# Kernel tuning notes

Hardware: AMD Instinct MI355X
Metric: run time of the kernel (lower is better)

## Reference

```python
import jax, jax.numpy as jnp
from jax import lax
import numpy as np

B, S, D_IN, D_OUT, LAT, N_STATE = 8, 2048, 1024, 1024, 256, 32
D_INNER, D_CONV, DT_RANK, N_BLK = 2 * D_OUT, 4, D_OUT // 16, 2


def setup_inputs() -> dict:
    key = jax.random.key(0)
    ks = iter(jax.random.split(key, 24))
    r = lambda shp, s=0.02: jax.random.normal(next(ks), shp, dtype=jnp.float32) * s
    inp = {
        "x": jax.random.normal(next(ks), (B, S, D_IN), dtype=jnp.float32),
        "W_in": r((D_IN, D_OUT)), "b_in": jnp.zeros((D_OUT,), jnp.float32),
        "Wa1": r((D_OUT, LAT)), "ba1": jnp.zeros((LAT,), jnp.float32),
        "Wa2": r((LAT, LAT)), "ba2": jnp.zeros((LAT,), jnp.float32),
        # per-block params, leading axis = N_BLK
        "gamma": jnp.ones((N_BLK, D_OUT), jnp.float32),
        "in_proj_w": r((N_BLK, D_OUT, 2 * D_INNER)),
        "conv_w": r((N_BLK, D_INNER, D_CONV), 0.1),
        "conv_b": jnp.zeros((N_BLK, D_INNER), jnp.float32),
        "x_proj_w": r((N_BLK, D_INNER, DT_RANK + 2 * N_STATE)),
        "dt_proj_w": r((N_BLK, DT_RANK, D_INNER), 0.1),
        "dt_proj_b": jnp.full((N_BLK, D_INNER), -4.6, jnp.float32),  # softplus(-4.6)~0.01
        "A_log": jnp.log(jnp.broadcast_to(jnp.arange(1, N_STATE + 1, dtype=jnp.float32), (N_BLK, D_INNER, N_STATE))),
        "D": jnp.ones((N_BLK, D_INNER), jnp.float32),
        "out_proj_w": r((N_BLK, D_INNER, D_OUT)),
    }
    return inp


def rms_norm(x, gamma):
    # F.normalize(x, dim=-1) * sqrt(d) * gamma
    norm = jnp.sqrt(jnp.sum(x * x, axis=-1, keepdims=True))
    return x / jnp.maximum(norm, 1e-12) * (x.shape[-1] ** 0.5) * gamma


def causal_conv1d(x, w, b):
    # x: [b, d, L], w: [d, d_conv] depthwise, causal (left) padding
    y = lax.conv_general_dilated(
        x, w[:, None, :], window_strides=(1,), padding=[(D_CONV - 1, 0)],
        feature_group_count=x.shape[1], dimension_numbers=("NCH", "OIH", "NCH"))
    return y + b[None, :, None]


def selective_scan(dA, dBu, C):
    # dA, dBu: [b, L, d_inner, n], C: [b, L, n] -> y: [b, L, d_inner]
    def step(h, inp):
        dA_t, dBu_t, C_t = inp
        h = dA_t * h + dBu_t
        return h, jnp.einsum("bdn,bn->bd", h, C_t)
    h0 = jnp.zeros(dA.shape[:1] + dA.shape[2:], dA.dtype)
    _, ys = lax.scan(step, h0, (dA.swapaxes(0, 1), dBu.swapaxes(0, 1), C.swapaxes(0, 1)))
    return ys.swapaxes(0, 1)


def mamba(u, in_w, cw, cb, xw, dtw, dtb, A_log, Dp, ow):
    # u: [b, L, d_model]
    xz = u @ in_w                              # [b, L, 2*d_inner]
    xh, z = jnp.split(xz, 2, axis=-1)
    xh = causal_conv1d(xh.swapaxes(1, 2), cw, cb).swapaxes(1, 2)
    xh = jax.nn.silu(xh)                       # [b, L, d_inner]
    xdbc = xh @ xw                             # [b, L, dt_rank + 2n]
    dt, Bm, Cm = jnp.split(xdbc, [DT_RANK, DT_RANK + N_STATE], axis=-1)
    dt = jax.nn.softplus(dt @ dtw + dtb)       # [b, L, d_inner]
    A = -jnp.exp(A_log)                        # [d_inner, n]
    dA = jnp.exp(dt[..., None] * A)            # [b, L, d_inner, n]
    dBu = dt[..., None] * Bm[:, :, None, :] * xh[..., None]
    y = selective_scan(dA, dBu, Cm) + Dp * xh
    y = y * jax.nn.silu(z)
    return y @ ow


def reference(x, W_in, b_in, Wa1, ba1, Wa2, ba2, gamma, in_proj_w, conv_w,
              conv_b, x_proj_w, dt_proj_w, dt_proj_b, A_log, D, out_proj_w):
    out = x @ W_in + b_in                      # [b, s, d]
    length = out.shape[1]
    w = jax.nn.silu(out @ Wa1 + ba1) @ Wa2 + ba2   # [b, s, LAT]
    w1 = jax.nn.softmax(w, axis=-1) * (LAT / length)
    w2 = jax.nn.softmax(w, axis=-2)
    weights = (w1 + w2) * 0.5
    out = jnp.einsum("bsd,bsS->bSd", out, weights)  # [b, LAT, d]
    for i in range(N_BLK):  # residual RMSNorm + Mamba (dropout = identity in eval)
        out = out + mamba(rms_norm(out, gamma[i]), in_proj_w[i], conv_w[i],
                          conv_b[i], x_proj_w[i], dt_proj_w[i], dt_proj_b[i],
                          A_log[i], D[i], out_proj_w[i])
    return out
```

## Files before the change

kernel.cpp:

```cpp
#include <hip/hip_runtime.h>
#include <math.h>
#include <stdint.h>

#define BB 8
#define SS 2048
#define D_IN 1024
#define D_OUTC 1024
#define LATC 256
#define NSTATE 32
#define DINNER 2048
#define DCONV 4
#define DTRANK 64
#define NCH 32

__device__ __forceinline__ float silu_f(float v) { return v * (1.f / (1.f + __expf(-v))); }
__device__ __forceinline__ float softplus_f(float v) {
    return fmaxf(v, 0.f) + log1pf(__expf(-fabsf(v)));
}

typedef short short8 __attribute__((ext_vector_type(8)));
typedef float f32x4 __attribute__((ext_vector_type(4)));

__device__ __forceinline__ unsigned short f2bf(float f) {
    unsigned u = __builtin_bit_cast(unsigned, f);
    u += 0x7FFFu + ((u >> 16) & 1u);
    return (unsigned short)(u >> 16);
}
__device__ __forceinline__ int pack2(float a, float b) {
    return (int)((unsigned)f2bf(a) | ((unsigned)f2bf(b) << 16));
}

typedef const __attribute__((address_space(1))) unsigned int* gas_ptr;
typedef __attribute__((address_space(3))) unsigned int* las_ptr;
__device__ __forceinline__ void gload16(const void* g, void* l) {
    __builtin_amdgcn_global_load_lds(
        reinterpret_cast<gas_ptr>(reinterpret_cast<uintptr_t>(g)),
        reinterpret_cast<las_ptr>(reinterpret_cast<uintptr_t>(l)),
        16, 0, 0);
}

__global__ __launch_bounds__(256) void transp_bf(const float* __restrict__ src,
                                                 unsigned short* __restrict__ dst,
                                                 int K, int N, long zsrc, long zdst)
{
    __shared__ float tile[32][33];
    src += (size_t)blockIdx.z * zsrc;
    dst += (size_t)blockIdx.z * zdst;
    const int n0 = blockIdx.x * 32;
    const int k0 = blockIdx.y * 32;
    const int x = threadIdx.x & 31;
    const int y = threadIdx.x >> 5;
#pragma unroll
    for (int j = 0; j < 4; j++)
        tile[y + 8 * j][x] = src[(size_t)(k0 + y + 8 * j) * N + n0 + x];
    __syncthreads();
#pragma unroll
    for (int j = 0; j < 4; j++)
        dst[(size_t)(n0 + y + 8 * j) * K + k0 + x] = f2bf(tile[x][y + 8 * j]);
}

__global__ __launch_bounds__(256) void transp16(const unsigned short* __restrict__ src,
                                                unsigned short* __restrict__ dst,
                                                int K, int N, long zsrc, long zdst)
{
    __shared__ unsigned short tile[32][33];
    src += (size_t)blockIdx.z * zsrc;
    dst += (size_t)blockIdx.z * zdst;
    const int n0 = blockIdx.x * 32;
    const int k0 = blockIdx.y * 32;
    const int x = threadIdx.x & 31;
    const int y = threadIdx.x >> 5;
#pragma unroll
    for (int j = 0; j < 4; j++)
        tile[y + 8 * j][x] = src[(size_t)(k0 + y + 8 * j) * N + n0 + x];
    __syncthreads();
#pragma unroll
    for (int j = 0; j < 4; j++)
        dst[(size_t)(n0 + y + 8 * j) * K + k0 + x] = tile[x][y + 8 * j];
}

__global__ __launch_bounds__(256) void cvt_bf16(const float* __restrict__ in,
                                                unsigned short* __restrict__ out)
{
    size_t i = ((size_t)blockIdx.x * 256 + threadIdx.x) * 8;
    float4 a = *(const float4*)(in + i);
    float4 b = *(const float4*)(in + i + 4);
    int4 w;
    w.x = pack2(a.x, a.y); w.y = pack2(a.z, a.w);
    w.z = pack2(b.x, b.y); w.w = pack2(b.z, b.w);
    *(int4*)(out + i) = w;
}

__global__ __launch_bounds__(256) void gemm16(
    const unsigned short* __restrict__ A, int lda,
    const unsigned short* __restrict__ BT, int ldb,
    const float* __restrict__ bias,
    float* __restrict__ C, int ldc,
    unsigned short* __restrict__ C16, int ldc16,
    int M, int N, int K, int act, int accum,
    int kspl, long zA, long zB, long zC, long zK)
{
    __shared__ __align__(16) unsigned short As[2][128 * 32];
    __shared__ __align__(16) unsigned short Bs[2][128 * 32];

    const int bz = blockIdx.z / kspl;
    const int ks = blockIdx.z % kspl;
    A += (size_t)bz * zA + (size_t)ks * (size_t)K;
    BT += (size_t)bz * zB + (size_t)ks * (size_t)K;
    if (C) C += (size_t)bz * zC + (size_t)ks * zK;

    const int tid = threadIdx.x;
    const int lane = tid & 63;
    const int wave = tid >> 6;
    const int wr = wave >> 1;
    const int wc = wave & 1;
    const int quad = lane >> 4;
    const int l16 = lane & 15;

    const int nbx = gridDim.x;
    const int nwg = nbx * gridDim.y;
    const int orig = blockIdx.y * nbx + blockIdx.x;
    const int q = nwg >> 3, r = nwg & 7;
    const int xcd = orig & 7, lid = orig >> 3;
    const int swz = (xcd < r) ? (xcd * (q + 1) + lid)
                              : (r * (q + 1) + (xcd - r) * q + lid);
    const int m0 = (swz / nbx) * 128;
    const int n0 = (swz % nbx) * 128;

    const int srow4 = lane >> 2;
    const int sphys = lane & 3;

    f32x4 acc[4][4];
#pragma unroll
    for (int i = 0; i < 4; i++)
#pragma unroll
        for (int j = 0; j < 4; j++) acc[i][j] = (f32x4){0.f, 0.f, 0.f, 0.f};

    const int nt = K >> 5;

    auto STAGE = [&](int buf, int t) {
        const int k0 = t << 5;
#pragma unroll
        for (int i = 0; i < 2; i++) {
            const int rbase = (wave << 5) + (i << 4);
            const int rr = rbase + srow4;
            const int ls = sphys ^ ((rr >> 1) & 3);
            gload16(A + (size_t)(m0 + rr) * lda + (k0 + (ls << 3)), &As[buf][rbase << 5]);
            gload16(BT + (size_t)(n0 + rr) * ldb + (k0 + (ls << 3)), &Bs[buf][rbase << 5]);
        }
    };

    STAGE(0, 0);
    asm volatile("s_waitcnt vmcnt(0)" ::: "memory");
    __syncthreads();

    int cur = 0;
    for (int t = 0; t < nt; ++t) {
        if (t + 1 < nt) STAGE(cur ^ 1, t + 1);

        short8 af[4], bfr[4];
#pragma unroll
        for (int i = 0; i < 4; i++) {
            const int ar = (wr << 6) + (i << 4) + l16;
            af[i] = *(const short8*)&As[cur][(ar << 5) + ((quad ^ ((ar >> 1) & 3)) << 3)];
            const int br = (wc << 6) + (i << 4) + l16;
            bfr[i] = *(const short8*)&Bs[cur][(br << 5) + ((quad ^ ((br >> 1) & 3)) << 3)];
        }
#pragma unroll
        for (int i = 0; i < 4; i++)
#pragma unroll
            for (int j = 0; j < 4; j++)
                acc[i][j] = __builtin_amdgcn_mfma_f32_16x16x32_bf16(af[i], bfr[j], acc[i][j], 0, 0, 0);

        asm volatile("s_waitcnt vmcnt(0)" ::: "memory");
        __syncthreads();
        cur ^= 1;
    }

#pragma unroll
    for (int j = 0; j < 4; j++) {
        int gn = n0 + wc * 64 + j * 16 + l16;
        float bv = bias ? bias[gn] : 0.f;
#pragma unroll
        for (int i = 0; i < 4; i++) {
#pragma unroll
            for (int r2 = 0; r2 < 4; r2++) {
                int gm = m0 + wr * 64 + i * 16 + quad * 4 + r2;
                float v = acc[i][j][r2] + bv;
                if (act == 1) v = silu_f(v);
                else if (act == 2) v = softplus_f(v);
                if (C) {
                    size_t ci = (size_t)gm * ldc + gn;
                    if (accum) C[ci] += v;
                    else C[ci] = v;
                }
                if (C16) C16[(size_t)gm * ldc16 + gn] = f2bf(v);
            }
        }
    }
}

__global__ __launch_bounds__(256) void gemm_kernel(
    const float* __restrict__ A, int lda, long strideA,
    const float* __restrict__ B, int ldb, long strideB,
    const float* __restrict__ bias,
    float* __restrict__ C, int ldc, long strideC,
    int M, int N, int K, int transA, int act, int accum)
{
    __shared__ float As[16][65];
    __shared__ float Bsh[16][64];

    const int bz = blockIdx.z;
    const float* Ab = A + (size_t)bz * strideA;
    const float* Bb = B + (size_t)bz * strideB;
    float* Cb = C + (size_t)bz * strideC;

    const int tx = threadIdx.x;
    const int ty = threadIdx.y;
    const int tid = ty * 16 + tx;
    const int m0 = blockIdx.y * 64;
    const int n0 = blockIdx.x * 64;

    float acc[4][4];
#pragma unroll
    for (int i = 0; i < 4; i++)
#pragma unroll
        for (int j = 0; j < 4; j++) acc[i][j] = 0.f;

    for (int k0 = 0; k0 < K; k0 += 16) {
        if (!transA) {
            int row = tid >> 2;
            int kc = (tid & 3) * 4;
            int gm = m0 + row;
#pragma unroll
            for (int j = 0; j < 4; j++) {
                int gk = k0 + kc + j;
                As[kc + j][row] = (gm < M && gk < K) ? Ab[(size_t)gm * lda + gk] : 0.f;
            }
        } else {
            int krow = tid >> 4;
            int mc = (tid & 15) * 4;
            int gk = k0 + krow;
#pragma unroll
            for (int j = 0; j < 4; j++) {
                int gm = m0 + mc + j;
                As[krow][mc + j] = (gm < M && gk < K) ? Ab[(size_t)gk * lda + gm] : 0.f;
            }
        }
        {
            int krow = tid >> 4;
            int nc = (tid & 15) * 4;
            int gk = k0 + krow;
#pragma unroll
            for (int j = 0; j < 4; j++) {
                int gn = n0 + nc + j;
                Bsh[krow][nc + j] = (gk < K && gn < N) ? Bb[(size_t)gk * ldb + gn] : 0.f;
            }
        }
        __syncthreads();
#pragma unroll
        for (int k = 0; k < 16; k++) {
            float a[4], bv[4];
#pragma unroll
            for (int i = 0; i < 4; i++) a[i] = As[k][ty * 4 + i];
#pragma unroll
            for (int j = 0; j < 4; j++) bv[j] = Bsh[k][tx * 4 + j];
#pragma unroll
            for (int i = 0; i < 4; i++)
#pragma unroll
                for (int j = 0; j < 4; j++) acc[i][j] += a[i] * bv[j];
        }
        __syncthreads();
    }

#pragma unroll
    for (int i = 0; i < 4; i++) {
        int gm = m0 + ty * 4 + i;
        if (gm >= M) continue;
#pragma unroll
        for (int j = 0; j < 4; j++) {
            int gn = n0 + tx * 4 + j;
            if (gn >= N) continue;
            float v = acc[i][j];
            if (bias) v += bias[gn];
            if (act == 1) v = silu_f(v);
            else if (act == 2) v = softplus_f(v);
            size_t ci = (size_t)gm * ldc + gn;
            if (accum) Cb[ci] += v;
            else Cb[ci] = v;
        }
    }
}

__global__ __launch_bounds__(256) void merge4_kernel(const float* __restrict__ part,
                                                     float* __restrict__ out, int n)
{
    int i = blockIdx.x * 256 + threadIdx.x;
    out[i] = part[i] + part[i + n] + part[i + 2 * n] + part[i + 3 * n];
}

__global__ __launch_bounds__(256) void merge2_kernel(const float* __restrict__ part,
                                                     float* __restrict__ out, int n)
{
    int i = blockIdx.x * 256 + threadIdx.x;
    out[i] = part[i] + part[i + n];
}

__global__ __launch_bounds__(256) void colstats_part_kernel(const float* __restrict__ w,
                                                            float* __restrict__ part)
{
    int b = blockIdx.x / NCH;
    int ch = blockIdx.x % NCH;
    int l = threadIdx.x;
    const float* base = w + ((size_t)b * SS + (size_t)ch * (SS / NCH)) * LATC + l;
    float m = -1e30f, s = 0.f;
    for (int t = 0; t < SS / NCH; t++) {
        float v = base[(size_t)t * LATC];
        float nm = fmaxf(m, v);
        s = s * __expf(m - nm) + __expf(v - nm);
        m = nm;
    }
    float2* p = (float2*)part;
    p[(size_t)(b * LATC + l) * NCH + ch] = make_float2(m, s);
}

__global__ __launch_bounds__(256) void colstats_merge_kernel(const float* __restrict__ part,
                                                             float* __restrict__ colst)
{
    int idx = blockIdx.x * 256 + threadIdx.x;
    const float2* p = (const float2*)part + (size_t)idx * NCH;
    float m = -1e30f, s = 0.f;
#pragma unroll 4
    for (int c = 0; c < NCH; c++) {
        float2 v = p[c];
        float nm = fmaxf(m, v.x);
        s = s * __expf(m - nm) + v.y * __expf(v.x - nm);
        m = nm;
    }
    colst[idx * 2] = m;
    colst[idx * 2 + 1] = s;
}

__global__ __launch_bounds__(256) void softmix_kernel(float* __restrict__ w,
                                                      const float* __restrict__ colst)
{
    int bs = blockIdx.x;
    int b = bs / SS;
    int l = threadIdx.x;
    float* row = w + (size_t)bs * LATC;
    float v = row[l];

    __shared__ float sm[256];
    sm[l] = v;
    __syncthreads();
    for (int st = 128; st > 0; st >>= 1) {
        if (l < st) sm[l] = fmaxf(sm[l], sm[l + st]);
        __syncthreads();
    }
    float rmax = sm[0];
    __syncthreads();
    float e = __expf(v - rmax);
    sm[l] = e;
    __syncthreads();
    for (int st = 128; st > 0; st >>= 1) {
        if (l < st) sm[l] += sm[l + st];
        __syncthreads();
    }
    float rsum = sm[0];

    float w1 = e / rsum * ((float)LATC / (float)SS);
    float cm = colst[(b * LATC + l) * 2];
    float cs = colst[(b * LATC + l) * 2 + 1];
    float w2 = __expf(v - cm) / cs;
    row[l] = 0.5f * (w1 + w2);
}

__global__ __launch_bounds__(256) void rmsnorm_kernel(const float* __restrict__ x,
                                                      const float* __restrict__ gamma,
                                                      unsigned short* __restrict__ out)
{
    int row = blockIdx.x;
    const float* xr = x + (size_t)row * D_OUTC;
    float v[4];
    float ss = 0.f;
#pragma unroll
    for (int i = 0; i < 4; i++) {
        v[i] = xr[threadIdx.x + i * 256];
        ss += v[i] * v[i];
    }
#pragma unroll
    for (int off = 32; off >= 1; off >>= 1) ss += __shfl_xor(ss, off, 64);
    __shared__ float sred[4];
    int wave = threadIdx.x >> 6;
    if ((threadIdx.x & 63) == 0) sred[wave] = ss;
    __syncthreads();
    float tot = sred[0] + sred[1] + sred[2] + sred[3];
    float inv = 32.0f / fmaxf(sqrtf(tot), 1e-12f);
    unsigned short* outr = out + (size_t)row * D_OUTC;
#pragma unroll
    for (int i = 0; i < 4; i++) {
        int d = threadIdx.x + i * 256;
        outr[d] = f2bf(v[i] * inv * gamma[d]);
    }
}

__global__ __launch_bounds__(256) void conv_silu_kernel(const float* __restrict__ xz,
                                                        const float* __restrict__ cw,
                                                        const float* __restrict__ cb,
                                                        float* __restrict__ xh, int L)
{
    int idx = blockIdx.x * 256 + threadIdx.x;
    int c = idx % DINNER;
    int bl = idx / DINNER;
    int l = bl % L;
    int b = bl / L;
    float acc = cb[c];
#pragma unroll
    for (int j = 0; j < DCONV; j++) {
        int ls = l - (DCONV - 1) + j;
        if (ls >= 0)
            acc += xz[((size_t)(b * L + ls)) * (2 * DINNER) + c] * cw[c * DCONV + j];
    }
    xh[idx] = silu_f(acc);
}

#define SCH 4
__global__ __launch_bounds__(256) void scan_kernel(const float* __restrict__ dty,
                                                   const float* __restrict__ xh,
                                                   const float* __restrict__ xz,
                                                   const float* __restrict__ xdbc,
                                                   const float* __restrict__ A_log,
                                                   const float* __restrict__ Dp,
                                                   unsigned short* __restrict__ ybf,
                                                   int L)
{
    const int t = threadIdx.x;
    const int g = t & 7;
    const int dloc = t >> 3;
    const int b = blockIdx.x >> 6;
    const int d = ((blockIdx.x & 63) << 5) + dloc;

    float4 Av = *(const float4*)(A_log + (size_t)d * NSTATE + g * 4);
    const float A0 = -__expf(Av.x), A1 = -__expf(Av.y), A2 = -__expf(Av.z), A3 = -__expf(Av.w);
    float h0 = 0.f, h1 = 0.f, h2 = 0.f, h3 = 0.f;
    const float Dd = Dp[d];

    const float* pdt = dty + (size_t)b * L * DINNER + d;
    const float* pxh = xh + (size_t)b * L * DINNER + d;
    const float* pz  = xz + (size_t)b * L * 2 * DINNER + DINNER + d;
    const float* pbc = xdbc + (size_t)b * L * 128 + DTRANK + g * 4;
    unsigned short* pout = ybf + (size_t)b * L * DINNER + d;

    float a_dt[SCH], a_x[SCH], a_z[SCH];
    float4 a_B[SCH], a_C[SCH];
    float n_dt[SCH], n_x[SCH], n_z[SCH];
    float4 n_B[SCH], n_C[SCH];

#pragma unroll
    for (int j = 0; j < SCH; j++) {
        a_dt[j] = pdt[(size_t)j * DINNER];
        a_x[j]  = pxh[(size_t)j * DINNER];
        a_z[j]  = pz[(size_t)j * 2 * DINNER];
        a_B[j]  = *(const float4*)(pbc + (size_t)j * 128);
        a_C[j]  = *(const float4*)(pbc + (size_t)j * 128 + NSTATE);
    }

    for (int l0 = 0; l0 < L; l0 += SCH) {
        const int lb = (l0 + SCH < L) ? (l0 + SCH) : l0;
#pragma unroll
        for (int j = 0; j < SCH; j++) {
            n_dt[j] = pdt[(size_t)(lb + j) * DINNER];
            n_x[j]  = pxh[(size_t)(lb + j) * DINNER];
            n_z[j]  = pz[(size_t)(lb + j) * 2 * DINNER];
            n_B[j]  = *(const float4*)(pbc + (size_t)(lb + j) * 128);
            n_C[j]  = *(const float4*)(pbc + (size_t)(lb + j) * 128 + NSTATE);
        }
#pragma unroll
        for (int j = 0; j < SCH; j++) {
            float dtv = a_dt[j], xv = a_x[j], zv = a_z[j];
            float dtx = dtv * xv;
            float e0 = __expf(dtv * A0);
            float e1 = __expf(dtv * A1);
            float e2 = __expf(dtv * A2);
            float e3 = __expf(dtv * A3);
            h0 = e0 * h0 + dtx * a_B[j].x;
            h1 = e1 * h1 + dtx * a_B[j].y;
            h2 = e2 * h2 + dtx * a_B[j].z;
            h3 = e3 * h3 + dtx * a_B[j].w;
            float accv = h0 * a_C[j].x + h1 * a_C[j].y + h2 * a_C[j].z + h3 * a_C[j].w;
            accv += __shfl_xor(accv, 1, 64);
            accv += __shfl_xor(accv, 2, 64);
            accv += __shfl_xor(accv, 4, 64);
            if (g == 0) {
                float yv = (accv + Dd * xv) * silu_f(zv);
                pout[(size_t)(l0 + j) * DINNER] = f2bf(yv);
            }
        }
#pragma unroll
        for (int j = 0; j < SCH; j++) {
            a_dt[j] = n_dt[j]; a_x[j] = n_x[j]; a_z[j] = n_z[j];
            a_B[j] = n_B[j];   a_C[j] = n_C[j];
        }
    }
}


extern "C" void kernel_launch(void* const* d_in, const int* in_sizes, int n_in,
                              void* d_out, int out_size, void* d_ws, size_t ws_size,
                              hipStream_t stream)
{
    const float* x      = (const float*)d_in[0];
    const float* W_in   = (const float*)d_in[1];
    const float* b_in   = (const float*)d_in[2];
    const float* Wa1    = (const float*)d_in[3];
    const float* ba1    = (const float*)d_in[4];
    const float* Wa2    = (const float*)d_in[5];
    const float* ba2    = (const float*)d_in[6];
    const float* gamma  = (const float*)d_in[7];
    const float* in_w   = (const float*)d_in[8];
    const float* conv_w = (const float*)d_in[9];
    const float* conv_b = (const float*)d_in[10];
    const float* x_w    = (const float*)d_in[11];
    const float* dt_w   = (const float*)d_in[12];
    const float* dt_b   = (const float*)d_in[13];
    const float* A_log  = (const float*)d_in[14];
    const float* Dp     = (const float*)d_in[15];
    const float* out_w  = (const float*)d_in[16];
    float* latout = (float*)d_out;

    char* wsb = (char*)d_ws;
    const size_t MB = 1 << 20;

    unsigned short* out0_bf = (unsigned short*)(wsb);
    unsigned short* xbf     = (unsigned short*)(wsb + 32 * MB);
    float*          wbuf    = (float*)(wsb + 64 * MB);
    unsigned short* t1_bf   = (unsigned short*)(wsb + 80 * MB);
    unsigned short* WinT    = (unsigned short*)(wsb + 88 * MB);
    unsigned short* Wa1T    = (unsigned short*)(wsb + 90 * MB);
    unsigned short* Wa2T    = (unsigned short*)(wsb + 90 * MB + 512 * 1024);
    float*          cs_part = (float*)(wsb + 91 * MB);
    float*          colst   = (float*)(wsb + 95 * MB);

    unsigned short* out0T   = (unsigned short*)(wsb + 32 * MB);
    unsigned short* wT      = (unsigned short*)(wsb + 80 * MB);
    float*          part6   = (float*)(wsb + 64 * MB);

    unsigned short* unorm_bf  = (unsigned short*)(wsb);
    float*          xdbc_part = (float*)(wsb + 4 * MB);
    float*          dtbuf     = (float*)(wsb + 8 * MB);
    unsigned short* ybf       = (unsigned short*)(wsb + 24 * MB);
    float*          xz        = (float*)(wsb + 32 * MB);
    float*          xh        = (float*)(wsb + 64 * MB);
    unsigned short* wprojT    = (unsigned short*)(wsb + 80 * MB);
    unsigned short* oprojT    = (unsigned short*)(wsb + 88 * MB);
    float*          xdbc      = (float*)(wsb + 92 * MB);

    dim3 blk(16, 16);
    const int L = LATC;
    const int M1 = BB * SS;
    const int ML = BB * L;

    cvt_bf16<<<dim3((size_t)M1 * D_IN / 2048), dim3(256), 0, stream>>>(x, xbf);
    transp_bf<<<dim3(D_OUTC / 32, D_IN / 32), dim3(256), 0, stream>>>(W_in, WinT, D_IN, D_OUTC, 0, 0);
    transp_bf<<<dim3(LATC / 32, D_OUTC / 32), dim3(256), 0, stream>>>(Wa1, Wa1T, D_OUTC, LATC, 0, 0);
    transp_bf<<<dim3(LATC / 32, LATC / 32), dim3(256), 0, stream>>>(Wa2, Wa2T, LATC, LATC, 0, 0);

    gemm16<<<dim3(D_OUTC / 128, M1 / 128), dim3(256), 0, stream>>>(
        xbf, D_IN, WinT, D_IN, b_in, (float*)nullptr, 0, out0_bf, D_OUTC,
        M1, D_OUTC, D_IN, 0, 0, 1, 0, 0, 0, 0);

    gemm16<<<dim3(LATC / 128, M1 / 128), dim3(256), 0, stream>>>(
        out0_bf, D_OUTC, Wa1T, D_OUTC, ba1, (float*)nullptr, 0, t1_bf, LATC,
        M1, LATC, D_OUTC, 1, 0, 1, 0, 0, 0, 0);

    gemm16<<<dim3(LATC / 128, M1 / 128), dim3(256), 0, stream>>>(
        t1_bf, LATC, Wa2T, LATC, ba2, wbuf, LATC, (unsigned short*)nullptr, 0,
        M1, LATC, LATC, 0, 0, 1, 0, 0, 0, 0);

    colstats_part_kernel<<<dim3(BB * NCH), dim3(256), 0, stream>>>(wbuf, cs_part);
    colstats_merge_kernel<<<dim3(BB * LATC / 256), dim3(256), 0, stream>>>(cs_part, colst);
    softmix_kernel<<<dim3(BB * SS), dim3(256), 0, stream>>>(wbuf, colst);

    transp16<<<dim3(D_OUTC / 32, SS / 32, BB), dim3(256), 0, stream>>>(
        out0_bf, out0T, SS, D_OUTC, (long)SS * D_OUTC, (long)D_OUTC * SS);
    transp_bf<<<dim3(LATC / 32, SS / 32, BB), dim3(256), 0, stream>>>(
        wbuf, wT, SS, LATC, (long)SS * LATC, (long)LATC * SS);
    gemm16<<<dim3(D_OUTC / 128, LATC / 128, BB * 2), dim3(256), 0, stream>>>(
        wT, SS, out0T, SS, (const float*)nullptr,
        part6, D_OUTC, (unsigned short*)nullptr, 0,
        LATC, D_OUTC, SS / 2, 0, 0,
        2, (long)LATC * SS, (long)D_OUTC * SS, (long)LATC * D_OUTC,
        (long)BB * LATC * D_OUTC);
    merge2_kernel<<<dim3(BB * LATC * D_OUTC / 256), dim3(256), 0, stream>>>(
        part6, latout, BB * LATC * D_OUTC);

    for (int i = 0; i < 2; i++) {
        const float* in_wi = in_w + (size_t)i * D_OUTC * 2 * DINNER;
        const float* cwi = conv_w + (size_t)i * DINNER * DCONV;
        const float* cbi = conv_b + (size_t)i * DINNER;
        const float* xwi = x_w + (size_t)i * DINNER * (DTRANK + 2 * NSTATE);
        const float* dtwi = dt_w + (size_t)i * DTRANK * DINNER;
        const float* dtbi = dt_b + (size_t)i * DINNER;
        const float* Ali = A_log + (size_t)i * DINNER * NSTATE;
        const float* Dpi = Dp + (size_t)i * DINNER;
        const float* owi = out_w + (size_t)i * DINNER * D_OUTC;
        const float* gi = gamma + (size_t)i * D_OUTC;

        transp_bf<<<dim3(2 * DINNER / 32, D_OUTC / 32), dim3(256), 0, stream>>>(
            in_wi, wprojT, D_OUTC, 2 * DINNER, 0, 0);
        transp_bf<<<dim3(D_OUTC / 32, DINNER / 32), dim3(256), 0, stream>>>(
            owi, oprojT, DINNER, D_OUTC, 0, 0);

        rmsnorm_kernel<<<dim3(ML), dim3(256), 0, stream>>>(latout, gi, unorm_bf);

        gemm16<<<dim3(2 * DINNER / 128, ML / 128), dim3(256), 0, stream>>>(
            unorm_bf, D_OUTC, wprojT, D_OUTC, (const float*)nullptr,
            xz, 2 * DINNER, (unsigned short*)nullptr, 0,
            ML, 2 * DINNER, D_OUTC, 0, 0, 1, 0, 0, 0, 0);

        conv_silu_kernel<<<dim3(BB * L * DINNER / 256), dim3(256), 0, stream>>>(xz, cwi, cbi, xh, L);

        gemm_kernel<<<dim3(128 / 64, ML / 64, 4), blk, 0, stream>>>(
            xh, DINNER, 512, xwi, 128, (long)512 * 128, (const float*)nullptr,
            xdbc_part, 128, (long)ML * 128, ML, 128, 512, 0, 0, 0);
        merge4_kernel<<<dim3(ML * 128 / 256), dim3(256), 0, stream>>>(
            xdbc_part, xdbc, ML * 128);

        gemm_kernel<<<dim3(DINNER / 64, ML / 64, 1), blk, 0, stream>>>(
            xdbc, 128, 0, dtwi, DINNER, 0, dtbi, dtbuf, DINNER, 0, ML, DINNER, DTRANK, 0, 2, 0);

        scan_kernel<<<dim3(BB * DINNER * 8 / 256), dim3(256), 0, stream>>>(
            dtbuf, xh, xz, xdbc, Ali, Dpi, ybf, L);

        gemm16<<<dim3(D_OUTC / 128, ML / 128), dim3(256), 0, stream>>>(
            ybf, DINNER, oprojT, DINNER, (const float*)nullptr,
            latout, D_OUTC, (unsigned short*)nullptr, 0,
            ML, D_OUTC, DINNER, 0, 1, 1, 0, 0, 0, 0);
    }
}
```

Measured before the change: 995.7 us.

## Split selective scan into chunked three-pass parallel scan over sequence

The sequential scan over the 256-step latent sequence is replaced by three passes. The first computes per-chunk final states and summed dt for 4 chunks in parallel. A small kernel then propagates the carried states across chunks. The scan is re-run per chunk starting from the propagated state. This gives 4x more blocks and a 4x shorter serial dependency chain, at the cost of reading dt/x/B twice and extra launches. Scratch buffers reuse workspace regions that held the in-proj weights and the normalized input.

```diff
diff --git a/kernel.cpp b/kernel.cpp
--- a/kernel.cpp
+++ b/kernel.cpp
@@ -425,12 +425,104 @@
 }
 
 #define SCH 4
+#define NCHS 4
+#define CHL (LATC / NCHS)
+
+__global__ __launch_bounds__(256) void scan_prop(const float* __restrict__ dty,
+                                                 const float* __restrict__ xh,
+                                                 const float* __restrict__ xdbc,
+                                                 const float* __restrict__ A_log,
+                                                 float* __restrict__ hfin,
+                                                 float* __restrict__ sdtb,
+                                                 int L)
+{
+    const int t = threadIdx.x;
+    const int g = t & 7;
+    const int dloc = t >> 3;
+    const int b = blockIdx.x >> 6;
+    const int d = ((blockIdx.x & 63) << 5) + dloc;
+    const int c = blockIdx.y;
+
+    float4 Av = *(const float4*)(A_log + (size_t)d * NSTATE + g * 4);
+    const float A0 = -__expf(Av.x), A1 = -__expf(Av.y), A2 = -__expf(Av.z), A3 = -__expf(Av.w);
+    float h0 = 0.f, h1 = 0.f, h2 = 0.f, h3 = 0.f, sdt = 0.f;
+
+    const float* pdt = dty + ((size_t)b * L + (size_t)c * CHL) * DINNER + d;
+    const float* pxh = xh + ((size_t)b * L + (size_t)c * CHL) * DINNER + d;
+    const float* pbc = xdbc + ((size_t)b * L + (size_t)c * CHL) * 128 + DTRANK + g * 4;
+
+    float a_dt[SCH], a_x[SCH];
+    float4 a_B[SCH];
+    float n_dt[SCH], n_x[SCH];
+    float4 n_B[SCH];
+
+#pragma unroll
+    for (int j = 0; j < SCH; j++) {
+        a_dt[j] = pdt[(size_t)j * DINNER];
+        a_x[j]  = pxh[(size_t)j * DINNER];
+        a_B[j]  = *(const float4*)(pbc + (size_t)j * 128);
+    }
+
+    for (int l0 = 0; l0 < CHL; l0 += SCH) {
+        const int lb = (l0 + SCH < CHL) ? (l0 + SCH) : l0;
+#pragma unroll
+        for (int j = 0; j < SCH; j++) {
+            n_dt[j] = pdt[(size_t)(lb + j) * DINNER];
+            n_x[j]  = pxh[(size_t)(lb + j) * DINNER];
+            n_B[j]  = *(const float4*)(pbc + (size_t)(lb + j) * 128);
+        }
+#pragma unroll
+        for (int j = 0; j < SCH; j++) {
+            float dtv = a_dt[j];
+            float dtx = dtv * a_x[j];
+            sdt += dtv;
+            float e0 = __expf(dtv * A0);
+            float e1 = __expf(dtv * A1);
+            float e2 = __expf(dtv * A2);
+            float e3 = __expf(dtv * A3);
+            h0 = e0 * h0 + dtx * a_B[j].x;
+            h1 = e1 * h1 + dtx * a_B[j].y;
+            h2 = e2 * h2 + dtx * a_B[j].z;
+            h3 = e3 * h3 + dtx * a_B[j].w;
+        }
+#pragma unroll
+        for (int j = 0; j < SCH; j++) {
+            a_dt[j] = n_dt[j]; a_x[j] = n_x[j]; a_B[j] = n_B[j];
+        }
+    }
+
+    float4 hv; hv.x = h0; hv.y = h1; hv.z = h2; hv.w = h3;
+    *(float4*)(hfin + ((((size_t)b * NCHS + c) * DINNER + d) << 5) + g * 4) = hv;
+    if (g == 0) sdtb[((size_t)b * NCHS + c) * DINNER + d] = sdt;
+}
+
+__global__ __launch_bounds__(256) void scan_mid(float* __restrict__ hfin,
+                                                const float* __restrict__ sdtb,
+                                                const float* __restrict__ A_log)
+{
+    int idx = blockIdx.x * 256 + threadIdx.x;
+    int n = idx & 31;
+    int d = (idx >> 5) & (DINNER - 1);
+    int b = idx >> 16;
+    float An = -__expf(A_log[(size_t)d * NSTATE + n]);
+    float h = 0.f;
+#pragma unroll
+    for (int c = 0; c < NCHS; c++) {
+        size_t slot = ((((size_t)b * NCHS + c) * DINNER + d) << 5) + n;
+        float hf = hfin[slot];
+        hfin[slot] = h;
+        float S = sdtb[((size_t)b * NCHS + c) * DINNER + d];
+        h = __expf(An * S) * h + hf;
+    }
+}
+
 __global__ __launch_bounds__(256) void scan_kernel(const float* __restrict__ dty,
                                                    const float* __restrict__ xh,
                                                    const float* __restrict__ xz,
                                                    const float* __restrict__ xdbc,
                                                    const float* __restrict__ A_log,
                                                    const float* __restrict__ Dp,
+                                                   const float* __restrict__ hin,
                                                    unsigned short* __restrict__ ybf,
                                                    int L)
 {
@@ -439,17 +531,19 @@
     const int dloc = t >> 3;
     const int b = blockIdx.x >> 6;
     const int d = ((blockIdx.x & 63) << 5) + dloc;
+    const int c = blockIdx.y;
 
     float4 Av = *(const float4*)(A_log + (size_t)d * NSTATE + g * 4);
     const float A0 = -__expf(Av.x), A1 = -__expf(Av.y), A2 = -__expf(Av.z), A3 = -__expf(Av.w);
-    float h0 = 0.f, h1 = 0.f, h2 = 0.f, h3 = 0.f;
+    float4 hv = *(const float4*)(hin + ((((size_t)b * NCHS + c) * DINNER + d) << 5) + g * 4);
+    float h0 = hv.x, h1 = hv.y, h2 = hv.z, h3 = hv.w;
     const float Dd = Dp[d];
 
-    const float* pdt = dty + (size_t)b * L * DINNER + d;
-    const float* pxh = xh + (size_t)b * L * DINNER + d;
-    const float* pz  = xz + (size_t)b * L * 2 * DINNER + DINNER + d;
-    const float* pbc = xdbc + (size_t)b * L * 128 + DTRANK + g * 4;
-    unsigned short* pout = ybf + (size_t)b * L * DINNER + d;
+    const float* pdt = dty + ((size_t)b * L + (size_t)c * CHL) * DINNER + d;
+    const float* pxh = xh + ((size_t)b * L + (size_t)c * CHL) * DINNER + d;
+    const float* pz  = xz + ((size_t)b * L + (size_t)c * CHL) * 2 * DINNER + DINNER + d;
+    const float* pbc = xdbc + ((size_t)b * L + (size_t)c * CHL) * 128 + DTRANK + g * 4;
+    unsigned short* pout = ybf + ((size_t)b * L + (size_t)c * CHL) * DINNER + d;
 
     float a_dt[SCH], a_x[SCH], a_z[SCH];
     float4 a_B[SCH], a_C[SCH];
@@ -465,8 +559,8 @@
         a_C[j]  = *(const float4*)(pbc + (size_t)j * 128 + NSTATE);
     }
 
-    for (int l0 = 0; l0 < L; l0 += SCH) {
-        const int lb = (l0 + SCH < L) ? (l0 + SCH) : l0;
+    for (int l0 = 0; l0 < CHL; l0 += SCH) {
+        const int lb = (l0 + SCH < CHL) ? (l0 + SCH) : l0;
 #pragma unroll
         for (int j = 0; j < SCH; j++) {
             n_dt[j] = pdt[(size_t)(lb + j) * DINNER];
@@ -554,6 +648,8 @@
     unsigned short* wprojT    = (unsigned short*)(wsb + 80 * MB);
     unsigned short* oprojT    = (unsigned short*)(wsb + 88 * MB);
     float*          xdbc      = (float*)(wsb + 92 * MB);
+    float*          hfin      = (float*)(wsb + 80 * MB);
+    float*          sdtb      = (float*)(wsb);
 
     dim3 blk(16, 16);
     const int L = LATC;
@@ -629,8 +725,12 @@
         gemm_kernel<<<dim3(DINNER / 64, ML / 64, 1), blk, 0, stream>>>(
             xdbc, 128, 0, dtwi, DINNER, 0, dtbi, dtbuf, DINNER, 0, ML, DINNER, DTRANK, 0, 2, 0);
 
-        scan_kernel<<<dim3(BB * DINNER * 8 / 256), dim3(256), 0, stream>>>(
-            dtbuf, xh, xz, xdbc, Ali, Dpi, ybf, L);
+        scan_prop<<<dim3(BB * 64, NCHS), dim3(256), 0, stream>>>(
+            dtbuf, xh, xdbc, Ali, hfin, sdtb, L);
+        scan_mid<<<dim3(BB * DINNER * NSTATE / 256), dim3(256), 0, stream>>>(
+            hfin, sdtb, Ali);
+        scan_kernel<<<dim3(BB * 64, NCHS), dim3(256), 0, stream>>>(
+            dtbuf, xh, xz, xdbc, Ali, Dpi, hfin, ybf, L);
 
         gemm16<<<dim3(D_OUTC / 128, ML / 128), dim3(256), 0, stream>>>(
             ybf, DINNER, oprojT, DINNER, (const float*)nullptr,
```

After: 1.008 ms. Within noise of the previous version (+1.2%).
